# Kernel tuning notes

Measured on AMD Instinct MI355X. Metric: run time of the kernel, lower is better.

## Reference

```python
import jax, jax.numpy as jnp
import numpy as np

B, H, W, C = 8, 128, 128, 256
NH = 8
HD = C // NH
WS = 8           # window size
SS = 4           # shift size
N = WS * WS      # tokens per window
SCALE = HD ** -0.5
EPS = 1e-5


def _rel_pos_index():
    coords = np.stack(np.meshgrid(np.arange(WS), np.arange(WS), indexing='ij'))  # [2,WS,WS]
    cf = coords.reshape(2, -1)                                                   # [2,N]
    rel = (cf[:, :, None] - cf[:, None, :]).transpose(1, 2, 0)                   # [N,N,2]
    rel[..., 0] += WS - 1
    rel[..., 1] += WS - 1
    rel[..., 0] *= 2 * WS - 1
    return rel.sum(-1)  # [N,N] indices into (2*WS-1)^2 table

RPI = jnp.asarray(_rel_pos_index())


def _attn_mask():
    img = np.zeros((H, W))
    slices = (slice(0, -WS), slice(-WS, -SS), slice(-SS, None))
    cnt = 0
    for hs in slices:
        for ws_ in slices:
            img[hs, ws_] = cnt
            cnt += 1
    mw = img.reshape(H // WS, WS, W // WS, WS).transpose(0, 2, 1, 3).reshape(-1, N)  # [nW,N]
    am = mw[:, None, :] - mw[:, :, None]
    return jnp.asarray(np.where(am != 0, -100.0, 0.0).astype(np.float32))  # [nW,N,N]

ATTN_MASK = _attn_mask()


def _ln(x, g, b):
    m = jnp.mean(x, -1, keepdims=True)
    v = jnp.var(x, -1, keepdims=True)
    return (x - m) * jax.lax.rsqrt(v + EPS) * g + b


def setup_inputs() -> dict:
    key = jax.random.key(0)
    ks = jax.random.split(key, 8)
    s = 0.02
    return {
        'x': jax.random.normal(ks[0], (B, H * W, C), jnp.float32),
        'qkv_w': jax.random.normal(ks[1], (C, 3 * C), jnp.float32) * s,
        'qkv_b': jnp.zeros((3 * C,), jnp.float32),
        'proj_w': jax.random.normal(ks[2], (C, C), jnp.float32) * s,
        'proj_b': jnp.zeros((C,), jnp.float32),
        'rpb': jax.random.normal(ks[3], ((2 * WS - 1) ** 2, NH), jnp.float32) * s,
        'g1': jnp.ones((C,), jnp.float32), 'b1': jnp.zeros((C,), jnp.float32),
        'g2': jnp.ones((C,), jnp.float32), 'b2': jnp.zeros((C,), jnp.float32),
        'fc1_w': jax.random.normal(ks[4], (C, 4 * C), jnp.float32) * s,
        'fc1_b': jnp.zeros((4 * C,), jnp.float32),
        'fc2_w': jax.random.normal(ks[5], (4 * C, C), jnp.float32) * s,
        'fc2_b': jnp.zeros((C,), jnp.float32),
    }


def reference(x, qkv_w, qkv_b, proj_w, proj_b, rpb, g1, b1, g2, b2,
              fc1_w, fc1_b, fc2_w, fc2_b):
    nW = (H // WS) * (W // WS)
    shortcut = x
    h = _ln(x, g1, b1).reshape(B, H, W, C)
    # cyclic shift
    h = jnp.roll(h, (-SS, -SS), axis=(1, 2))
    # window partition -> (B*nW, N, C)
    win = h.reshape(B, H // WS, WS, W // WS, WS, C).transpose(0, 1, 3, 2, 4, 5).reshape(-1, N, C)
    qkv = (win @ qkv_w + qkv_b).reshape(-1, N, 3, NH, HD).transpose(2, 0, 3, 1, 4)  # [3,B_,NH,N,HD]
    q, k, v = qkv[0] * SCALE, qkv[1], qkv[2]
    attn = jnp.einsum('bhnd,bhmd->bhnm', q, k)                    # [B_,NH,N,N]
    bias = rpb[RPI].transpose(2, 0, 1)                             # [NH,N,N]
    attn = attn + bias[None]
    attn = attn.reshape(B, nW, NH, N, N) + ATTN_MASK[None, :, None]
    attn = jax.nn.softmax(attn.reshape(-1, NH, N, N), axis=-1)
    out = jnp.einsum('bhnm,bhmd->bhnd', attn, v).transpose(0, 2, 1, 3).reshape(-1, N, C)
    out = out @ proj_w + proj_b
    # window reverse + reverse shift
    out = out.reshape(B, H // WS, W // WS, WS, WS, C).transpose(0, 1, 3, 2, 4, 5).reshape(B, H, W, C)
    out = jnp.roll(out, (SS, SS), axis=(1, 2)).reshape(B, H * W, C)
    x = shortcut + out
    hm = _ln(x, g2, b2)
    hm = jax.nn.gelu(hm @ fc1_w + fc1_b, approximate=False) @ fc2_w + fc2_b
    return x + hm
```

## Files before the change

### kernel.cpp

```cpp
#include <hip/hip_runtime.h>
#include <math.h>


#define NWIN_TOTAL 2048
#define TOK_TOTAL  131072
#define SCALE_Q    0.17677669529663687f
#define LOG2E      1.4426950408889634f

typedef unsigned short u16;
typedef __attribute__((ext_vector_type(4))) unsigned short u16x4;
typedef __attribute__((ext_vector_type(8))) unsigned short u16x8;
typedef __attribute__((ext_vector_type(8))) short bf16x8;
typedef __attribute__((ext_vector_type(4))) float f32x4;

#define AS1 __attribute__((address_space(1)))
#define AS3 __attribute__((address_space(3)))
#define GLOAD_LDS16(g, l) \
  __builtin_amdgcn_global_load_lds((const AS1 unsigned int*)(g), (AS3 unsigned int*)(l), 16, 0, 0)

__device__ __forceinline__ float bf2f(u16 u) {
  union { unsigned int i; float f; } c; c.i = ((unsigned int)u) << 16; return c.f;
}
__device__ __forceinline__ u16 f2bf(float f) {
  union { float f; unsigned int i; } c; c.f = f;
  return (u16)((c.i + 0x7fff + ((c.i >> 16) & 1)) >> 16);
}
__device__ __forceinline__ int regid3(int h) { return h < 120 ? 0 : (h < 124 ? 1 : 2); }
__device__ __forceinline__ float gelu_f(float v) {
  float t = exp2f(v * fmaf(v * v, 0.10294423f, 2.3022082f));
  return v * t * __builtin_amdgcn_rcpf(t + 1.0f);
}

__device__ __forceinline__ int win_tok_to_t(int g, int n) {
  int b = g >> 8, wi = g & 255;
  int wr = wi >> 4, wc = wi & 15;
  int hs = wr * 8 + (n >> 3), ws2 = wc * 8 + (n & 7);
  int h = (hs + 4) & 127, w = (ws2 + 4) & 127;
  return (b << 14) + (h << 7) + w;
}

__global__ __launch_bounds__(256)
void wconv_kernel(const float* __restrict__ w, u16* __restrict__ wt, int K, int N)
{
  int i = blockIdx.x * 256 + threadIdx.x;
  if (i >= K * N) return;
  int k = i / N, n = i - k * N;
  wt[(size_t)n * K + k] = f2bf(w[i]);
}

__global__ __launch_bounds__(1024)
void qln_kernel(const float* __restrict__ x, const float* __restrict__ g1,
                const float* __restrict__ b1, const u16* __restrict__ qkvT,
                const float* __restrict__ qkv_b,
                u16* __restrict__ qb, u16* __restrict__ kb, u16* __restrict__ vb,
                int g0)
{
  __shared__ u16 Aln[16384];
  const int tid = threadIdx.x, wid = tid >> 6, lane = tid & 63;
  const int l15 = lane & 15, g = lane >> 4;
  const int bwi = blockIdx.x;
  const int gw = g0 + bwi;

  {
    const int row = tid >> 4;
    const int cq = (tid & 15) * 16;
    const int t = win_tok_to_t(gw, row);
    const float* src = x + (size_t)t * 256 + cq;
    float vals[16];
    float s = 0.f, q = 0.f;
#pragma unroll
    for (int i = 0; i < 4; ++i) {
      float4 v = ((const float4*)src)[i];
      vals[i*4] = v.x; vals[i*4+1] = v.y; vals[i*4+2] = v.z; vals[i*4+3] = v.w;
      s += v.x + v.y + v.z + v.w;
      q += v.x*v.x + v.y*v.y + v.z*v.z + v.w*v.w;
    }
    s += __shfl_xor(s, 1, 64); q += __shfl_xor(q, 1, 64);
    s += __shfl_xor(s, 2, 64); q += __shfl_xor(q, 2, 64);
    s += __shfl_xor(s, 4, 64); q += __shfl_xor(q, 4, 64);
    s += __shfl_xor(s, 8, 64); q += __shfl_xor(q, 8, 64);
    float mean = s * 0.00390625f;
    float rstd = rsqrtf(q * 0.00390625f - mean * mean + 1e-5f);
#pragma unroll
    for (int i = 0; i < 2; ++i) {
      const int col = cq + i * 8;
      u16x8 o;
#pragma unroll
      for (int j = 0; j < 8; ++j)
        o[j] = f2bf((vals[i*8+j] - mean) * rstd * g1[col+j] + b1[col+j]);
      const int gran = col >> 3;
      *(u16x8*)((char*)Aln + row * 512 + ((gran ^ (row & 7)) << 4)) = o;
    }
  }
  __syncthreads();

  f32x4 acc[4][3];
#pragma unroll
  for (int m = 0; m < 4; ++m)
#pragma unroll
    for (int n = 0; n < 3; ++n) acc[m][n] = (f32x4){0.f, 0.f, 0.f, 0.f};
  const int colb = wid * 48;
#pragma unroll
  for (int ks = 0; ks < 8; ++ks) {
    bf16x8 af[4], bw[3];
#pragma unroll
    for (int m = 0; m < 4; ++m) {
      const int tok = m * 16 + l15;
      const int gran = ks * 4 + g;
      af[m] = *(const bf16x8*)&Aln[tok * 256 + ((gran ^ (tok & 7)) << 3)];
    }
#pragma unroll
    for (int n = 0; n < 3; ++n)
      bw[n] = *(const bf16x8*)(qkvT + (size_t)(colb + n * 16 + l15) * 256 + ks * 32 + g * 8);
#pragma unroll
    for (int m = 0; m < 4; ++m)
#pragma unroll
      for (int n = 0; n < 3; ++n)
        acc[m][n] = __builtin_amdgcn_mfma_f32_16x16x32_bf16(af[m], bw[n], acc[m][n], 0, 0, 0);
  }

#pragma unroll
  for (int n = 0; n < 3; ++n) {
    const int col16 = colb + n * 16;
    const float bv = qkv_b[col16 + l15];
    const int s = col16 >> 8, head = (col16 >> 5) & 7, hd = col16 & 31;
    if (s == 2) {
      const size_t obase = ((size_t)bwi << 14) + ((size_t)head << 11) + (size_t)(hd + l15) * 64;
#pragma unroll
      for (int m = 0; m < 4; ++m) {
        const int tok0 = m * 16 + g * 4;
        u16x4 pk;
#pragma unroll
        for (int r = 0; r < 4; ++r) pk[r] = f2bf(acc[m][n][r] + bv);
        *(u16x4*)&vb[obase + tok0] = pk;
      }
    } else {
      u16* qdst = (s == 0) ? qb : kb;
      const float scl = (s == 0) ? SCALE_Q * LOG2E : 1.f;
      const size_t obase = ((size_t)bwi << 14) + ((size_t)head << 11) + hd + l15;
#pragma unroll
      for (int m = 0; m < 4; ++m)
#pragma unroll
        for (int r = 0; r < 4; ++r) {
          const int tok = m * 16 + g * 4 + r;
          qdst[obase + ((size_t)tok << 5)] = f2bf((acc[m][n][r] + bv) * scl);
        }
    }
  }
}

__global__ __launch_bounds__(512)
void awp_kernel(const u16* __restrict__ qb, const u16* __restrict__ kb,
                const u16* __restrict__ vt, const float* __restrict__ rpb,
                const u16* __restrict__ pjT, const float* __restrict__ pjb,
                const float* __restrict__ x, float* __restrict__ out, int g0)
{
  __shared__ union {
    u16 pl[8][2048];
    u16 aoL[16384];
    float rep[8192];
  } sb;
  __shared__ float rl[1800];
  const int tid = threadIdx.x, hh = tid >> 6, lane = tid & 63;
  const int l15 = lane & 15, g = lane >> 4;
  const int bw = blockIdx.x;

  for (int i = tid; i < 1800; i += 512) {
    unsigned int h2 = (unsigned)i / 225u;
    unsigned int rem = (unsigned)i - h2 * 225u;
    unsigned int aa = rem / 15u, bb = rem - aa * 15u;
    rl[i] = rpb[(aa * 15u + 14u - bb) * 8u + h2] * LOG2E;
  }
  __syncthreads();

  const size_t base = ((size_t)(bw * 8 + hh)) << 11;

  bf16x8 qf[4], kf[4];
#pragma unroll
  for (int f = 0; f < 4; ++f) {
    qf[f] = *(const bf16x8*)(qb + base + (size_t)(f * 16 + l15) * 32 + g * 8);
    kf[f] = *(const bf16x8*)(kb + base + (size_t)(f * 16 + l15) * 32 + g * 8);
  }
  f32x4 acc[4][4];
#pragma unroll
  for (int mf = 0; mf < 4; ++mf)
#pragma unroll
    for (int nf = 0; nf < 4; ++nf) acc[mf][nf] = (f32x4){0.f, 0.f, 0.f, 0.f};
#pragma unroll
  for (int mf = 0; mf < 4; ++mf)
#pragma unroll
    for (int nf = 0; nf < 4; ++nf)
      acc[mf][nf] = __builtin_amdgcn_mfma_f32_16x16x32_bf16(kf[mf], qf[nf], acc[mf][nf], 0, 0, 0);

  const int gwin = g0 + bw;
  const int wrw = (gwin >> 4) & 15, wcw = gwin & 15;
  const bool edge = (wrw == 15) || (wcw == 15);
  const int i2b = g >> 1;
  const int j2b = (g & 1) * 4;
#pragma unroll
  for (int nf = 0; nf < 4; ++nf) {
    const int n = nf * 16 + l15;
    const int i1 = n >> 3, j1 = n & 7;
    const int rid1 = edge ? regid3(wrw * 8 + i1) * 3 + regid3(wcw * 8 + j1) : 0;
#pragma unroll
    for (int mf = 0; mf < 4; ++mf) {
      const int i2 = mf * 2 + i2b;
      const int ib = hh * 225 + (i1 - i2 + 7) * 15 + (j2b - j1 + 7);
      const int r2a = edge ? regid3(wrw * 8 + i2) * 3 : 0;
#pragma unroll
      for (int r = 0; r < 4; ++r) {
        float b = rl[ib + r];
        if (edge) {
          int rid2 = r2a + regid3(wcw * 8 + j2b + r);
          if (rid2 != rid1) b -= 144.2695f;
        }
        acc[mf][nf][r] += b;
      }
    }
  }

  float inv[4];
#pragma unroll
  for (int nf = 0; nf < 4; ++nf) {
    float m0 = -1e30f;
#pragma unroll
    for (int mf = 0; mf < 4; ++mf)
#pragma unroll
      for (int r = 0; r < 4; ++r) m0 = fmaxf(m0, acc[mf][nf][r]);
    m0 = fmaxf(m0, __shfl_xor(m0, 16, 64));
    m0 = fmaxf(m0, __shfl_xor(m0, 32, 64));
    float s = 0.f;
#pragma unroll
    for (int mf = 0; mf < 4; ++mf)
#pragma unroll
      for (int r = 0; r < 4; ++r) {
        float p = exp2f(acc[mf][nf][r] - m0);
        acc[mf][nf][r] = p;
        s += p;
      }
    s += __shfl_xor(s, 16, 64);
    s += __shfl_xor(s, 32, 64);
    inv[nf] = 1.f / s;
  }

  bf16x8 vf[2][2];
#pragma unroll
  for (int df = 0; df < 2; ++df)
#pragma unroll
    for (int ks = 0; ks < 2; ++ks)
      vf[df][ks] = *(const bf16x8*)(vt + base + (size_t)(df * 16 + l15) * 64 + ks * 32 + g * 8);
  f32x4 accO[4][2];
#pragma unroll
  for (int nf = 0; nf < 4; ++nf)
#pragma unroll
    for (int df = 0; df < 2; ++df) accO[nf][df] = (f32x4){0.f, 0.f, 0.f, 0.f};
  char* plw = (char*)sb.pl[hh];
#pragma unroll
  for (int ks = 0; ks < 2; ++ks) {
#pragma unroll
    for (int nf = 0; nf < 4; ++nf) {
      const int n = nf * 16 + l15;
      const int swz = (n & 3) << 4;
#pragma unroll
      for (int mm = 0; mm < 2; ++mm) {
        const int mf = ks * 2 + mm;
        float p0 = acc[mf][nf][0] * inv[nf], p1 = acc[mf][nf][1] * inv[nf];
        float p2 = acc[mf][nf][2] * inv[nf], p3 = acc[mf][nf][3] * inv[nf];
        unsigned int pa, pb;
        asm("v_cvt_pk_bf16_f32 %0, %1, %2" : "=v"(pa) : "v"(p0), "v"(p1));
        asm("v_cvt_pk_bf16_f32 %0, %1, %2" : "=v"(pb) : "v"(p2), "v"(p3));
        uint2 w; w.x = pa; w.y = pb;
        *(uint2*)(plw + ((n * 64 + mm * 32 + g * 8) ^ swz)) = w;
      }
    }
#pragma unroll
    for (int nf = 0; nf < 4; ++nf) {
      const int n = nf * 16 + l15;
      const int swz = (n & 3) << 4;
      bf16x8 pf = *(const bf16x8*)(plw + ((n * 64 + g * 16) ^ swz));
#pragma unroll
      for (int df = 0; df < 2; ++df)
        accO[nf][df] = __builtin_amdgcn_mfma_f32_16x16x32_bf16(pf, vf[df][ks], accO[nf][df], 0, 0, 0);
    }
  }

  __syncthreads();
#pragma unroll
  for (int nf = 0; nf < 4; ++nf)
#pragma unroll
    for (int r = 0; r < 4; ++r) {
      const int tok = nf * 16 + g * 4 + r;
#pragma unroll
      for (int df = 0; df < 2; ++df) {
        const int ch = hh * 32 + df * 16 + l15;
        *(u16*)((char*)sb.aoL + tok * 512 + ((((ch >> 3) ^ (tok & 7))) << 4) + (ch & 7) * 2) =
            f2bf(accO[nf][df][r]);
      }
    }
  __syncthreads();

  f32x4 pacc[4][2];
#pragma unroll
  for (int mf = 0; mf < 4; ++mf)
#pragma unroll
    for (int of = 0; of < 2; ++of) pacc[mf][of] = (f32x4){0.f, 0.f, 0.f, 0.f};
  const u16* pB = pjT + (size_t)(hh * 32) * 256;
#pragma unroll
  for (int ks = 0; ks < 8; ++ks) {
    bf16x8 af[4], bwf[2];
#pragma unroll
    for (int mf = 0; mf < 4; ++mf) {
      const int tok = mf * 16 + l15;
      af[mf] = *(const bf16x8*)((char*)sb.aoL + tok * 512 + (((ks * 4 + g) ^ (tok & 7)) << 4));
    }
#pragma unroll
    for (int of = 0; of < 2; ++of)
      bwf[of] = *(const bf16x8*)(pB + (size_t)(of * 16 + l15) * 256 + ks * 32 + g * 8);
#pragma unroll
    for (int mf = 0; mf < 4; ++mf)
#pragma unroll
      for (int of = 0; of < 2; ++of)
        pacc[mf][of] = __builtin_amdgcn_mfma_f32_16x16x32_bf16(af[mf], bwf[of], pacc[mf][of], 0, 0, 0);
  }

#pragma unroll
  for (int hp = 0; hp < 2; ++hp) {
    __syncthreads();
#pragma unroll
    for (int mm = 0; mm < 2; ++mm) {
      const int mf = hp * 2 + mm;
#pragma unroll
      for (int of = 0; of < 2; ++of) {
        const int oc = hh * 32 + of * 16 + l15;
        const float bv = pjb[oc];
#pragma unroll
        for (int r = 0; r < 4; ++r) {
          const int row = mm * 16 + g * 4 + r;
          *(float*)((char*)sb.rep + ((row * 1024 + oc * 4) ^ ((row & 3) << 4))) =
              pacc[mf][of][r] + bv;
        }
      }
    }
    __syncthreads();
    const int rowl = tid >> 4, coll = (tid & 15) * 16;
    const int tok = hp * 32 + rowl;
    const int t = win_tok_to_t(g0 + bw, tok);
    const float* xs = x + (size_t)t * 256 + coll;
    float* od = out + (size_t)t * 256 + coll;
#pragma unroll
    for (int i = 0; i < 4; ++i) {
      float4 rv = *(const float4*)((char*)sb.rep +
                    ((rowl * 1024 + (coll + i * 4) * 4) ^ ((rowl & 3) << 4)));
      float4 xv = ((const float4*)xs)[i];
      ((float4*)od)[i] = make_float4(rv.x + xv.x, rv.y + xv.y, rv.z + xv.z, rv.w + xv.w);
    }
  }
}

__global__ __launch_bounds__(512)
void mlp_kernel(float* io, const u16* __restrict__ w1t, const u16* __restrict__ w2t,
                const float* __restrict__ fb1, const float* __restrict__ fb2,
                const float* __restrict__ g2, const float* __restrict__ bt2)
{
  __shared__ u16 Aln[16384];
  __shared__ u16 Hs[8192];
  const int tid = threadIdx.x, wid = tid >> 6, lane = tid & 63;
  const int l15 = lane & 15, g = lane >> 4;
  const int t0 = blockIdx.x * 64;

  {
    const int row = tid >> 3;
    const int cq = (tid & 7) * 32;
    const float* src = io + (size_t)(t0 + row) * 256 + cq;
    float vals[32];
    float s = 0.f, q = 0.f;
#pragma unroll
    for (int i = 0; i < 8; ++i) {
      float4 v = ((const float4*)src)[i];
      vals[i*4] = v.x; vals[i*4+1] = v.y; vals[i*4+2] = v.z; vals[i*4+3] = v.w;
      s += v.x + v.y + v.z + v.w;
      q += v.x*v.x + v.y*v.y + v.z*v.z + v.w*v.w;
    }
    s += __shfl_xor(s, 1, 64); q += __shfl_xor(q, 1, 64);
    s += __shfl_xor(s, 2, 64); q += __shfl_xor(q, 2, 64);
    s += __shfl_xor(s, 4, 64); q += __shfl_xor(q, 4, 64);
    float mean = s * 0.00390625f;
    float rstd = rsqrtf(q * 0.00390625f - mean * mean + 1e-5f);
#pragma unroll
    for (int i = 0; i < 4; ++i) {
      const int col = cq + i * 8;
      u16x8 o;
#pragma unroll
      for (int j = 0; j < 8; ++j)
        o[j] = f2bf((vals[i*8+j] - mean) * rstd * g2[col+j] + bt2[col+j]);
      const int gran = col >> 3;
      *(u16x8*)((char*)Aln + row * 512 + ((gran ^ (row & 7)) << 4)) = o;
    }
  }
  __syncthreads();

  f32x4 acc2[4][2];
#pragma unroll
  for (int m = 0; m < 4; ++m)
#pragma unroll
    for (int n = 0; n < 2; ++n) acc2[m][n] = (f32x4){0.f, 0.f, 0.f, 0.f};

  for (int c = 0; c < 8; ++c) {
    f32x4 acc1[4];
#pragma unroll
    for (int tf = 0; tf < 4; ++tf) acc1[tf] = (f32x4){0.f, 0.f, 0.f, 0.f};
    const u16* w1base = w1t + (size_t)(c * 128 + wid * 16) * 256;
#pragma unroll
    for (int ks = 0; ks < 8; ++ks) {
      bf16x8 af = *(const bf16x8*)(w1base + (size_t)l15 * 256 + ks * 32 + g * 8);
      bf16x8 bfr[4];
#pragma unroll
      for (int tf = 0; tf < 4; ++tf) {
        const int tok = tf * 16 + l15;
        const int gran = ks * 4 + g;
        bfr[tf] = *(const bf16x8*)&Aln[tok * 256 + ((gran ^ (tok & 7)) << 3)];
      }
#pragma unroll
      for (int tf = 0; tf < 4; ++tf)
        acc1[tf] = __builtin_amdgcn_mfma_f32_16x16x32_bf16(af, bfr[tf], acc1[tf], 0, 0, 0);
    }
    __syncthreads();
    {
      const int hcl = wid * 16 + g * 4;
      const float b0 = fb1[c * 128 + hcl];
      const float b1 = fb1[c * 128 + hcl + 1];
      const float b2v = fb1[c * 128 + hcl + 2];
      const float b3 = fb1[c * 128 + hcl + 3];
#pragma unroll
      for (int tf = 0; tf < 4; ++tf) {
        const int tok = tf * 16 + l15;
        float p0 = gelu_f(acc1[tf][0] + b0);
        float p1 = gelu_f(acc1[tf][1] + b1);
        float p2 = gelu_f(acc1[tf][2] + b2v);
        float p3 = gelu_f(acc1[tf][3] + b3);
        unsigned int pa, pb;
        asm("v_cvt_pk_bf16_f32 %0, %1, %2" : "=v"(pa) : "v"(p0), "v"(p1));
        asm("v_cvt_pk_bf16_f32 %0, %1, %2" : "=v"(pb) : "v"(p2), "v"(p3));
        uint2 w; w.x = pa; w.y = pb;
        *(uint2*)((char*)Hs + tok * 256 + (((hcl >> 3) ^ (tok & 7)) << 4) + ((hcl & 4) << 1)) = w;
      }
    }
    __syncthreads();
    const u16* w2base = w2t + (size_t)(wid * 32) * 1024 + c * 128;
#pragma unroll
    for (int hk = 0; hk < 4; ++hk) {
      bf16x8 ah[4], bw[2];
#pragma unroll
      for (int tf = 0; tf < 4; ++tf) {
        const int tok = tf * 16 + l15;
        const int gran = hk * 4 + g;
        ah[tf] = *(const bf16x8*)&Hs[tok * 128 + ((gran ^ (tok & 7)) << 3)];
      }
#pragma unroll
      for (int of = 0; of < 2; ++of)
        bw[of] = *(const bf16x8*)(w2base + (size_t)(of * 16 + l15) * 1024 + hk * 32 + g * 8);
#pragma unroll
      for (int tf = 0; tf < 4; ++tf)
#pragma unroll
        for (int of = 0; of < 2; ++of)
          acc2[tf][of] = __builtin_amdgcn_mfma_f32_16x16x32_bf16(ah[tf], bw[of], acc2[tf][of], 0, 0, 0);
    }
  }

#pragma unroll
  for (int tf = 0; tf < 4; ++tf) {
#pragma unroll
    for (int of = 0; of < 2; ++of) {
      const int oc = wid * 32 + of * 16 + l15;
      const float bv = fb2[oc];
#pragma unroll
      for (int r = 0; r < 4; ++r) {
        const size_t off = (size_t)(t0 + tf * 16 + g * 4 + r) * 256 + oc;
        io[off] = acc2[tf][of][r] + bv + io[off];
      }
    }
  }
}

extern "C" void kernel_launch(void* const* d_in, const int* in_sizes, int n_in,
                              void* d_out, int out_size, void* d_ws, size_t ws_size,
                              hipStream_t stream)
{
  const float* x      = (const float*)d_in[0];
  const float* qkv_w  = (const float*)d_in[1];
  const float* qkv_b  = (const float*)d_in[2];
  const float* proj_w = (const float*)d_in[3];
  const float* proj_b = (const float*)d_in[4];
  const float* rpb    = (const float*)d_in[5];
  const float* g1     = (const float*)d_in[6];
  const float* b1     = (const float*)d_in[7];
  const float* g2     = (const float*)d_in[8];
  const float* b2     = (const float*)d_in[9];
  const float* fc1_w  = (const float*)d_in[10];
  const float* fc1_b  = (const float*)d_in[11];
  const float* fc2_w  = (const float*)d_in[12];
  const float* fc2_b  = (const float*)d_in[13];
  float* out = (float*)d_out;
  char* ws = (char*)d_ws;

  u16* qkvT  = (u16*)ws;
  u16* projT = qkvT + 196608;
  u16* fc1T  = projT + 65536;
  u16* fc2T  = fc1T + 262144;
  char* pb = (char*)(fc2T + 262144);
  size_t used = 1572864ULL;
  size_t R = ws_size > used ? ws_size - used : 0;

  wconv_kernel<<<(196608 + 255) / 256, 256, 0, stream>>>(qkv_w, qkvT, 256, 768);
  wconv_kernel<<<(65536  + 255) / 256, 256, 0, stream>>>(proj_w, projT, 256, 256);
  wconv_kernel<<<(262144 + 255) / 256, 256, 0, stream>>>(fc1_w, fc1T, 256, 1024);
  wconv_kernel<<<(262144 + 255) / 256, 256, 0, stream>>>(fc2_w, fc2T, 1024, 256);

  int Gc = 2048;
  while (Gc > 2 && (size_t)Gc * 98304ULL > R) Gc >>= 1;

  u16* qb = (u16*)pb;
  u16* kb = qb + (size_t)Gc * 16384;
  u16* vb = kb + (size_t)Gc * 16384;

  for (int g0 = 0; g0 < NWIN_TOTAL; g0 += Gc) {
    qln_kernel<<<Gc, 1024, 0, stream>>>(x, g1, b1, qkvT, qkv_b, qb, kb, vb, g0);
    awp_kernel<<<Gc, 512, 0, stream>>>(qb, kb, vb, rpb, projT, proj_b, x, out, g0);
  }

  mlp_kernel<<<TOK_TOTAL / 64, 512, 0, stream>>>(out, fc1T, fc2T, fc1_b, fc2_b, g2, b2);
}
```

Before: 651.6 us.

## Double-buffer MLP hidden tile and software-pipeline GEMM1/GEMM2 chunks

The MLP kernel now keeps two LDS buffers for the GELU hidden tile. Each iteration runs GEMM2 on the previous chunk and then GEMM1 plus GELU packing on the current chunk, which cuts the barriers from two per chunk to one and lets the two GEMMs' MFMA and load work interleave. It costs an extra 16KB of LDS per block, which may reduce occupancy, and the fully unrolled loop may raise register pressure.

Measured after the change: 640.9 us. About the same (-1.6%).

```diff
diff --git a/kernel.cpp b/kernel.cpp
--- a/kernel.cpp
+++ b/kernel.cpp
@@ -363,7 +363,7 @@
                 const float* __restrict__ g2, const float* __restrict__ bt2)
 {
   __shared__ u16 Aln[16384];
-  __shared__ u16 Hs[8192];
+  __shared__ u16 Hs[2][8192];
   const int tid = threadIdx.x, wid = tid >> 6, lane = tid & 63;
   const int l15 = lane & 15, g = lane >> 4;
   const int t0 = blockIdx.x * 64;
@@ -397,75 +397,97 @@
       *(u16x8*)((char*)Aln + row * 512 + ((gran ^ (row & 7)) << 4)) = o;
     }
   }
+
+  f32x4 acc2[4][2];
+#pragma unroll
+  for (int m = 0; m < 4; ++m)
+#pragma unroll
+    for (int n = 0; n < 2; ++n) acc2[m][n] = (f32x4){0.f, 0.f, 0.f, 0.f};
+  f32x4 acc1[4];
+
+#define MGEMM1(c)                                                                 \
+  {                                                                               \
+    _Pragma("unroll")                                                             \
+    for (int tf = 0; tf < 4; ++tf) acc1[tf] = (f32x4){0.f, 0.f, 0.f, 0.f};        \
+    const u16* w1base = w1t + (size_t)((c) * 128 + wid * 16) * 256;               \
+    _Pragma("unroll")                                                             \
+    for (int ks = 0; ks < 8; ++ks) {                                              \
+      bf16x8 af = *(const bf16x8*)(w1base + (size_t)l15 * 256 + ks * 32 + g * 8); \
+      bf16x8 bfr[4];                                                              \
+      _Pragma("unroll")                                                           \
+      for (int tf = 0; tf < 4; ++tf) {                                            \
+        const int tok = tf * 16 + l15;                                            \
+        const int gran = ks * 4 + g;                                              \
+        bfr[tf] = *(const bf16x8*)&Aln[tok * 256 + ((gran ^ (tok & 7)) << 3)];    \
+      }                                                                           \
+      _Pragma("unroll")                                                           \
+      for (int tf = 0; tf < 4; ++tf)                                              \
+        acc1[tf] = __builtin_amdgcn_mfma_f32_16x16x32_bf16(af, bfr[tf], acc1[tf], 0, 0, 0); \
+    }                                                                             \
+  }
+
+#define MPACK(c)                                                                  \
+  {                                                                               \
+    char* hdst = (char*)Hs[(c) & 1];                                              \
+    const int hcl = wid * 16 + g * 4;                                             \
+    const float b0 = fb1[(c) * 128 + hcl];                                        \
+    const float b1 = fb1[(c) * 128 + hcl + 1];                                    \
+    const float b2v = fb1[(c) * 128 + hcl + 2];                                   \
+    const float b3 = fb1[(c) * 128 + hcl + 3];                                    \
+    _Pragma("unroll")                                                             \
+    for (int tf = 0; tf < 4; ++tf) {                                              \
+      const int tok = tf * 16 + l15;                                              \
+      float p0 = gelu_f(acc1[tf][0] + b0);                                        \
+      float p1 = gelu_f(acc1[tf][1] + b1);                                        \
+      float p2 = gelu_f(acc1[tf][2] + b2v);                                       \
+      float p3 = gelu_f(acc1[tf][3] + b3);                                        \
+      unsigned int pa, pb;                                                        \
+      asm("v_cvt_pk_bf16_f32 %0, %1, %2" : "=v"(pa) : "v"(p0), "v"(p1));          \
+      asm("v_cvt_pk_bf16_f32 %0, %1, %2" : "=v"(pb) : "v"(p2), "v"(p3));          \
+      uint2 w; w.x = pa; w.y = pb;                                                \
+      *(uint2*)(hdst + tok * 256 + (((hcl >> 3) ^ (tok & 7)) << 4) + ((hcl & 4) << 1)) = w; \
+    }                                                                             \
+  }
+
+#define MGEMM2(c)                                                                 \
+  {                                                                               \
+    const u16* hsrc = Hs[(c) & 1];                                                \
+    const u16* w2base = w2t + (size_t)(wid * 32) * 1024 + (c) * 128;              \
+    _Pragma("unroll")                                                             \
+    for (int hk = 0; hk < 4; ++hk) {                                              \
+      bf16x8 ah[4], bw[2];                                                        \
+      _Pragma("unroll")                                                           \
+      for (int tf = 0; tf < 4; ++tf) {                                            \
+        const int tok = tf * 16 + l15;                                            \
+        const int gran = hk * 4 + g;                                              \
+        ah[tf] = *(const bf16x8*)&hsrc[tok * 128 + ((gran ^ (tok & 7)) << 3)];    \
+      }                                                                           \
+      _Pragma("unroll")                                                           \
+      for (int of = 0; of < 2; ++of)                                              \
+        bw[of] = *(const bf16x8*)(w2base + (size_t)(of * 16 + l15) * 1024 + hk * 32 + g * 8); \
+      _Pragma("unroll")                                                           \
+      for (int tf = 0; tf < 4; ++tf)                                              \
+        _Pragma("unroll")                                                         \
+        for (int of = 0; of < 2; ++of)                                            \
+          acc2[tf][of] = __builtin_amdgcn_mfma_f32_16x16x32_bf16(ah[tf], bw[of], acc2[tf][of], 0, 0, 0); \
+    }                                                                             \
+  }
+
   __syncthreads();
-
-  f32x4 acc2[4][2];
-#pragma unroll
-  for (int m = 0; m < 4; ++m)
-#pragma unroll
-    for (int n = 0; n < 2; ++n) acc2[m][n] = (f32x4){0.f, 0.f, 0.f, 0.f};
-
-  for (int c = 0; c < 8; ++c) {
-    f32x4 acc1[4];
-#pragma unroll
-    for (int tf = 0; tf < 4; ++tf) acc1[tf] = (f32x4){0.f, 0.f, 0.f, 0.f};
-    const u16* w1base = w1t + (size_t)(c * 128 + wid * 16) * 256;
-#pragma unroll
-    for (int ks = 0; ks < 8; ++ks) {
-      bf16x8 af = *(const bf16x8*)(w1base + (size_t)l15 * 256 + ks * 32 + g * 8);
-      bf16x8 bfr[4];
-#pragma unroll
-      for (int tf = 0; tf < 4; ++tf) {
-        const int tok = tf * 16 + l15;
-        const int gran = ks * 4 + g;
-        bfr[tf] = *(const bf16x8*)&Aln[tok * 256 + ((gran ^ (tok & 7)) << 3)];
-      }
-#pragma unroll
-      for (int tf = 0; tf < 4; ++tf)
-        acc1[tf] = __builtin_amdgcn_mfma_f32_16x16x32_bf16(af, bfr[tf], acc1[tf], 0, 0, 0);
-    }
+  MGEMM1(0);
+  MPACK(0);
+  __syncthreads();
+#pragma unroll
+  for (int c = 1; c < 8; ++c) {
+    MGEMM2(c - 1);
+    MGEMM1(c);
+    MPACK(c);
     __syncthreads();
-    {
-      const int hcl = wid * 16 + g * 4;
-      const float b0 = fb1[c * 128 + hcl];
-      const float b1 = fb1[c * 128 + hcl + 1];
-      const float b2v = fb1[c * 128 + hcl + 2];
-      const float b3 = fb1[c * 128 + hcl + 3];
-#pragma unroll
-      for (int tf = 0; tf < 4; ++tf) {
-        const int tok = tf * 16 + l15;
-        float p0 = gelu_f(acc1[tf][0] + b0);
-        float p1 = gelu_f(acc1[tf][1] + b1);
-        float p2 = gelu_f(acc1[tf][2] + b2v);
-        float p3 = gelu_f(acc1[tf][3] + b3);
-        unsigned int pa, pb;
-        asm("v_cvt_pk_bf16_f32 %0, %1, %2" : "=v"(pa) : "v"(p0), "v"(p1));
-        asm("v_cvt_pk_bf16_f32 %0, %1, %2" : "=v"(pb) : "v"(p2), "v"(p3));
-        uint2 w; w.x = pa; w.y = pb;
-        *(uint2*)((char*)Hs + tok * 256 + (((hcl >> 3) ^ (tok & 7)) << 4) + ((hcl & 4) << 1)) = w;
-      }
-    }
-    __syncthreads();
-    const u16* w2base = w2t + (size_t)(wid * 32) * 1024 + c * 128;
-#pragma unroll
-    for (int hk = 0; hk < 4; ++hk) {
-      bf16x8 ah[4], bw[2];
-#pragma unroll
-      for (int tf = 0; tf < 4; ++tf) {
-        const int tok = tf * 16 + l15;
-        const int gran = hk * 4 + g;
-        ah[tf] = *(const bf16x8*)&Hs[tok * 128 + ((gran ^ (tok & 7)) << 3)];
-      }
-#pragma unroll
-      for (int of = 0; of < 2; ++of)
-        bw[of] = *(const bf16x8*)(w2base + (size_t)(of * 16 + l15) * 1024 + hk * 32 + g * 8);
-#pragma unroll
-      for (int tf = 0; tf < 4; ++tf)
-#pragma unroll
-        for (int of = 0; of < 2; ++of)
-          acc2[tf][of] = __builtin_amdgcn_mfma_f32_16x16x32_bf16(ah[tf], bw[of], acc2[tf][of], 0, 0, 0);
-    }
-  }
+  }
+  MGEMM2(7);
+#undef MGEMM1
+#undef MPACK
+#undef MGEMM2
 
 #pragma unroll
   for (int tf = 0; tf < 4; ++tf) {
```
